# Performance work log

Measured on AMD Instinct MI355X. Metric: run time of the kernel, lower is better.

## Reference

```python
import jax, jax.numpy as jnp
import numpy as np

# _norm_l1l2l3(l1=1, l2=1, l3=2) = 3/4 (computed from the factorial/double-factorial formula)
NORM = 0.75

N, IN1, IN2, KOUT = 512, 128, 128, 128


def setup_inputs() -> dict:
    key = jax.random.key(0)
    k1, k2, k3 = jax.random.split(key, 3)
    x = jax.random.normal(k1, (N, 3, IN1), dtype=jnp.float32)
    y = jax.random.normal(k2, (N, 3, IN2), dtype=jnp.float32)
    w = jax.random.normal(k3, (IN1, IN2, KOUT), dtype=jnp.float32)
    a = jnp.float32(1.0)
    return {"w": w, "a": a, "x": x, "y": y}


def reference(w, a, x, y):
    # contraction1: outer product over the two Cartesian axes (l1=1, l2=1 -> l3=2)
    # x: [n, i=3, a], y: [n, j=3, b] -> out1: [n, 3, 3, a, b]
    out1 = jnp.einsum("nia,njb->nijab", x, y)
    # contraction2: weighted contraction of feature channels with scaled weights
    # (w*a): [a, b, k], out1: [n, 3, 3, a, b] -> [n, 3, 3, k]
    out2 = NORM * jnp.einsum("abk,nijab->nijk", w * a, out1)
    return (out1, out2)
```

## Files before the change

kernel.cpp:

```cpp
#include <hip/hip_runtime.h>
#include <stdint.h>

typedef __attribute__((ext_vector_type(8))) short bf16x8;
typedef __attribute__((ext_vector_type(4))) float f32x4;

static constexpr int O1_ELEMS    = 512*3*3*128*128;
static constexpr int WB2_FLOATS  = 1048576;
static constexpr size_t SCRATCH_BYTES = (size_t)WB2_FLOATS*4;
static constexpr int NTILES      = 4608;
static constexpr int SKIP_TILES  = 64;
static constexpr int S1          = 512;
static constexpr int NCB         = 384;

__device__ inline unsigned short f32_to_bf16(float f) {
    union { float f; uint32_t u; } v; v.f = f;
    uint32_t r = v.u + 0x7FFF + ((v.u >> 16) & 1);
    return (unsigned short)(r >> 16);
}

__device__ inline bf16x8 bf16x8_from_f32(const float* p) {
    float4 v0 = *(const float4*)p;
    float4 v1 = *(const float4*)(p + 4);
    union { bf16x8 v; unsigned short s[8]; } u;
    u.s[0] = f32_to_bf16(v0.x); u.s[1] = f32_to_bf16(v0.y);
    u.s[2] = f32_to_bf16(v0.z); u.s[3] = f32_to_bf16(v0.w);
    u.s[4] = f32_to_bf16(v1.x); u.s[5] = f32_to_bf16(v1.y);
    u.s[6] = f32_to_bf16(v1.z); u.s[7] = f32_to_bf16(v1.w);
    return u.v;
}

__device__ inline void write_tile(int tile, const float* __restrict__ x,
                                  const float* __restrict__ y,
                                  float* __restrict__ out1, int t) {
    const f32x4* y4 = (const f32x4*)y;
    f32x4* o4 = (f32x4*)out1;
    const int b4 = t & 31, a0 = t >> 5;
    int n  = tile / 9;
    int ij = tile - n * 9;
    int i  = ij / 3, j = ij - i * 3;
    f32x4 yv = y4[(n * 3 + j) * 32 + b4];
    const float* xrow = x + (n * 3 + i) * 128;
    f32x4* dst = o4 + (size_t)tile * 4096 + a0 * 32 + b4;
    #pragma unroll
    for (int p = 0; p < 16; ++p) {
        float xs = xrow[p * 8 + a0];
        f32x4 r = yv * xs;
        __builtin_nontemporal_store(r, dst);
        dst += 256;
    }
}

__device__ inline void conv_role(int a, int t, const float* __restrict__ w,
                                 unsigned short* __restrict__ wb2, char* smem) {
    unsigned short (*lt)[132] = (unsigned short (*)[132])smem;
    const float4* src = (const float4*)(w + (size_t)a * 16384);
    #pragma unroll
    for (int it = 0; it < 16; ++it) {
        int fidx = it * 256 + t;
        float4 v = src[fidx];
        int b = fidx >> 5, k4 = fidx & 31;
        unsigned short* d = &lt[b][k4 * 4];
        d[0] = f32_to_bf16(v.x); d[1] = f32_to_bf16(v.y);
        d[2] = f32_to_bf16(v.z); d[3] = f32_to_bf16(v.w);
    }
    __syncthreads();
    const int k = t >> 1, bh = t & 1;
    uint4* dst = (uint4*)(wb2 + (size_t)a * 16384 + (size_t)k * 128 + bh * 64);
    #pragma unroll
    for (int i8 = 0; i8 < 8; ++i8) {
        uint32_t pk[4];
        #pragma unroll
        for (int q = 0; q < 4; ++q) {
            uint32_t lo = lt[bh * 64 + i8 * 8 + q * 2][k];
            uint32_t hi = lt[bh * 64 + i8 * 8 + q * 2 + 1][k];
            pk[q] = lo | (hi << 16);
        }
        uint4 vv = {pk[0], pk[1], pk[2], pk[3]};
        dst[i8] = vv;
    }
}

__device__ inline void comp_role(int cb, int tid, float alpha,
                                 const float* __restrict__ x,
                                 const float* __restrict__ y,
                                 const unsigned short* __restrict__ wb2,
                                 float* __restrict__ out2, char* smem) {
    float (*xsh)[3][32] = (float (*)[3][32])smem;
    const int ksl = cb & 7;
    const int mt  = cb >> 3;
    const int l   = tid & 63;
    const int wv  = tid >> 6;
    const int l15 = l & 15, lg = l >> 4;

    bf16x8 afrag[2][4];
    #pragma unroll
    for (int Mt = 0; Mt < 2; ++Mt)
        #pragma unroll
        for (int ks = 0; ks < 4; ++ks)
            afrag[Mt][ks] = bf16x8_from_f32(
                y + (size_t)(mt * 32 + Mt * 16 + l15) * 128 + ks * 32 + lg * 8);

    #pragma unroll
    for (int p = 0; p < 48; ++p) {
        int e = tid + p * 256;
        int aa = e / 96, r = e - aa * 96, i = r >> 5, mm = r & 31;
        int n = (mt * 32 + mm) / 3;
        xsh[aa][i][mm] = x[n * 384 + i * 128 + aa];
    }
    __syncthreads();

    float acc2[3][2][4] = {};
    const unsigned short* wbase =
        wb2 + (size_t)(ksl * 16 + l15) * 128 + lg * 8;

    #pragma unroll 2
    for (int ac = 0; ac < 32; ++ac) {
        const int a = wv * 32 + ac;
        const unsigned short* wp = wbase + (size_t)a * 16384;
        bf16x8 bf0 = *(const bf16x8*)(wp);
        bf16x8 bf1 = *(const bf16x8*)(wp + 32);
        bf16x8 bf2 = *(const bf16x8*)(wp + 64);
        bf16x8 bf3 = *(const bf16x8*)(wp + 96);

        f32x4 t0 = {0.f, 0.f, 0.f, 0.f}, t1 = {0.f, 0.f, 0.f, 0.f};
        t0 = __builtin_amdgcn_mfma_f32_16x16x32_bf16(afrag[0][0], bf0, t0, 0, 0, 0);
        t1 = __builtin_amdgcn_mfma_f32_16x16x32_bf16(afrag[1][0], bf0, t1, 0, 0, 0);
        t0 = __builtin_amdgcn_mfma_f32_16x16x32_bf16(afrag[0][1], bf1, t0, 0, 0, 0);
        t1 = __builtin_amdgcn_mfma_f32_16x16x32_bf16(afrag[1][1], bf1, t1, 0, 0, 0);
        t0 = __builtin_amdgcn_mfma_f32_16x16x32_bf16(afrag[0][2], bf2, t0, 0, 0, 0);
        t1 = __builtin_amdgcn_mfma_f32_16x16x32_bf16(afrag[1][2], bf2, t1, 0, 0, 0);
        t0 = __builtin_amdgcn_mfma_f32_16x16x32_bf16(afrag[0][3], bf3, t0, 0, 0, 0);
        t1 = __builtin_amdgcn_mfma_f32_16x16x32_bf16(afrag[1][3], bf3, t1, 0, 0, 0);

        #pragma unroll
        for (int i = 0; i < 3; ++i) {
            float4 xv0 = *(const float4*)&xsh[a][i][lg * 4];
            float4 xv1 = *(const float4*)&xsh[a][i][16 + lg * 4];
            acc2[i][0][0] += xv0.x * t0[0]; acc2[i][0][1] += xv0.y * t0[1];
            acc2[i][0][2] += xv0.z * t0[2]; acc2[i][0][3] += xv0.w * t0[3];
            acc2[i][1][0] += xv1.x * t1[0]; acc2[i][1][1] += xv1.y * t1[1];
            acc2[i][1][2] += xv1.z * t1[2]; acc2[i][1][3] += xv1.w * t1[3];
        }
    }

    __syncthreads();
    float* red = (float*)smem;
    const int base = (wv * 64 + l) * 24;
    #pragma unroll
    for (int i = 0; i < 3; ++i)
        #pragma unroll
        for (int Mt = 0; Mt < 2; ++Mt)
            #pragma unroll
            for (int r = 0; r < 4; ++r)
                red[base + (i * 2 + Mt) * 4 + r] = acc2[i][Mt][r];
    __syncthreads();

    if (wv == 0) {
        #pragma unroll
        for (int i = 0; i < 3; ++i)
            #pragma unroll
            for (int Mt = 0; Mt < 2; ++Mt)
                #pragma unroll
                for (int r = 0; r < 4; ++r) {
                    const int idx = (i * 2 + Mt) * 4 + r;
                    float s = acc2[i][Mt][r]
                            + red[(64 + l) * 24 + idx]
                            + red[(128 + l) * 24 + idx]
                            + red[(192 + l) * 24 + idx];
                    int m = mt * 32 + Mt * 16 + lg * 4 + r;
                    int n = m / 3, j = m - 3 * n;
                    out2[((size_t)(n * 3 + i) * 3 + j) * 128 + ksl * 16 + l15] =
                        alpha * s;
                }
    }
}

__global__ __launch_bounds__(256) void k1_kernel(const float* __restrict__ w,
                                                 const float* __restrict__ x,
                                                 const float* __restrict__ y,
                                                 unsigned short* __restrict__ wb2,
                                                 float* __restrict__ out1, int t0) {
    __shared__ __align__(16) char smem[33792];
    const int b = (int)blockIdx.x;
    if (b < 128) { conv_role(b, (int)threadIdx.x, w, wb2, smem); return; }
    write_tile(t0 + b - 128, x, y, out1, (int)threadIdx.x);
}

__global__ __launch_bounds__(256) void k2_kernel(const float* __restrict__ a_s,
                                                 const float* __restrict__ x,
                                                 const float* __restrict__ y,
                                                 const unsigned short* __restrict__ wb2,
                                                 float* __restrict__ out1,
                                                 float* __restrict__ out2, int t0) {
    __shared__ __align__(16) char smem[49152];
    const int b = (int)blockIdx.x;
    const int t = (int)threadIdx.x;
    if (b < NCB) {
        comp_role(b, t, 0.75f * a_s[0], x, y, wb2, out2, smem);
        return;
    }
    write_tile(t0 + S1 + (b - NCB), x, y, out1, t);
}

__global__ __launch_bounds__(256) void finish_kernel(const float* __restrict__ x,
                                                     const float* __restrict__ y,
                                                     float* __restrict__ out1) {
    write_tile((int)blockIdx.x, x, y, out1, (int)threadIdx.x);
}

extern "C" void kernel_launch(void* const* d_in, const int* in_sizes, int n_in,
                              void* d_out, int out_size, void* d_ws, size_t ws_size,
                              hipStream_t stream) {
    const float* w  = (const float*)d_in[0];
    const float* as = (const float*)d_in[1];
    const float* x  = (const float*)d_in[2];
    const float* y  = (const float*)d_in[3];
    float* out1 = (float*)d_out;
    float* out2 = out1 + O1_ELEMS;

    const bool have_ws = (ws_size >= SCRATCH_BYTES);
    unsigned short* wb2 = have_ws ? (unsigned short*)d_ws : (unsigned short*)out1;
    const int t0 = have_ws ? 0 : SKIP_TILES;
    const int s2 = NTILES - t0 - S1;

    k1_kernel<<<128 + S1, 256, 0, stream>>>(w, x, y, wb2, out1, t0);
    k2_kernel<<<NCB + s2, 256, 0, stream>>>(as, x, y, wb2, out1, out2, t0);
    if (!have_ws)
        finish_kernel<<<SKIP_TILES, 256, 0, stream>>>(x, y, out1);
}
```

Baseline: 69.75 us.

## Fuse weight conversion into compute by gathering fp32 weights directly into MFMA fragments

Removes the separate bf16 transpose/convert pass over w and its scratch buffer, so the whole op becomes a single kernel launch. Compute blocks now read fp32 weights with strided scalar loads (stride 128 floats) and convert to bf16 in registers inside the MFMA loop. This drops one launch and a kernel boundary but replaces vector 16-byte loads with eight uncoalesced-per-lane scalar gathers per fragment, which increases load instructions and L2 traffic in the hot loop.

```diff
diff --git a/kernel.cpp b/kernel.cpp
--- a/kernel.cpp
+++ b/kernel.cpp
@@ -4,13 +4,9 @@
 typedef __attribute__((ext_vector_type(8))) short bf16x8;
 typedef __attribute__((ext_vector_type(4))) float f32x4;
 
-static constexpr int O1_ELEMS    = 512*3*3*128*128;
-static constexpr int WB2_FLOATS  = 1048576;
-static constexpr size_t SCRATCH_BYTES = (size_t)WB2_FLOATS*4;
-static constexpr int NTILES      = 4608;
-static constexpr int SKIP_TILES  = 64;
-static constexpr int S1          = 512;
-static constexpr int NCB         = 384;
+static constexpr int O1_ELEMS = 512*3*3*128*128;
+static constexpr int NTILES   = 4608;
+static constexpr int NCB      = 384;
 
 __device__ inline unsigned short f32_to_bf16(float f) {
     union { float f; uint32_t u; } v; v.f = f;
@@ -26,6 +22,13 @@
     u.s[2] = f32_to_bf16(v0.z); u.s[3] = f32_to_bf16(v0.w);
     u.s[4] = f32_to_bf16(v1.x); u.s[5] = f32_to_bf16(v1.y);
     u.s[6] = f32_to_bf16(v1.z); u.s[7] = f32_to_bf16(v1.w);
+    return u.v;
+}
+
+__device__ inline bf16x8 gather_bf16(const float* __restrict__ p) {
+    union { bf16x8 v; unsigned short s[8]; } u;
+    #pragma unroll
+    for (int q = 0; q < 8; ++q) u.s[q] = f32_to_bf16(p[q * 128]);
     return u.v;
 }
 
@@ -50,40 +53,10 @@
     }
 }
 
-__device__ inline void conv_role(int a, int t, const float* __restrict__ w,
-                                 unsigned short* __restrict__ wb2, char* smem) {
-    unsigned short (*lt)[132] = (unsigned short (*)[132])smem;
-    const float4* src = (const float4*)(w + (size_t)a * 16384);
-    #pragma unroll
-    for (int it = 0; it < 16; ++it) {
-        int fidx = it * 256 + t;
-        float4 v = src[fidx];
-        int b = fidx >> 5, k4 = fidx & 31;
-        unsigned short* d = &lt[b][k4 * 4];
-        d[0] = f32_to_bf16(v.x); d[1] = f32_to_bf16(v.y);
-        d[2] = f32_to_bf16(v.z); d[3] = f32_to_bf16(v.w);
-    }
-    __syncthreads();
-    const int k = t >> 1, bh = t & 1;
-    uint4* dst = (uint4*)(wb2 + (size_t)a * 16384 + (size_t)k * 128 + bh * 64);
-    #pragma unroll
-    for (int i8 = 0; i8 < 8; ++i8) {
-        uint32_t pk[4];
-        #pragma unroll
-        for (int q = 0; q < 4; ++q) {
-            uint32_t lo = lt[bh * 64 + i8 * 8 + q * 2][k];
-            uint32_t hi = lt[bh * 64 + i8 * 8 + q * 2 + 1][k];
-            pk[q] = lo | (hi << 16);
-        }
-        uint4 vv = {pk[0], pk[1], pk[2], pk[3]};
-        dst[i8] = vv;
-    }
-}
-
 __device__ inline void comp_role(int cb, int tid, float alpha,
                                  const float* __restrict__ x,
                                  const float* __restrict__ y,
-                                 const unsigned short* __restrict__ wb2,
+                                 const float* __restrict__ w,
                                  float* __restrict__ out2, char* smem) {
     float (*xsh)[3][32] = (float (*)[3][32])smem;
     const int ksl = cb & 7;
@@ -110,17 +83,16 @@
     __syncthreads();
 
     float acc2[3][2][4] = {};
-    const unsigned short* wbase =
-        wb2 + (size_t)(ksl * 16 + l15) * 128 + lg * 8;
+    const float* wgb = w + (size_t)(lg * 8) * 128 + ksl * 16 + l15;
 
     #pragma unroll 2
     for (int ac = 0; ac < 32; ++ac) {
         const int a = wv * 32 + ac;
-        const unsigned short* wp = wbase + (size_t)a * 16384;
-        bf16x8 bf0 = *(const bf16x8*)(wp);
-        bf16x8 bf1 = *(const bf16x8*)(wp + 32);
-        bf16x8 bf2 = *(const bf16x8*)(wp + 64);
-        bf16x8 bf3 = *(const bf16x8*)(wp + 96);
+        const float* wp = wgb + (size_t)a * 16384;
+        bf16x8 bf0 = gather_bf16(wp);
+        bf16x8 bf1 = gather_bf16(wp + 32 * 128);
+        bf16x8 bf2 = gather_bf16(wp + 64 * 128);
+        bf16x8 bf3 = gather_bf16(wp + 96 * 128);
 
         f32x4 t0 = {0.f, 0.f, 0.f, 0.f}, t1 = {0.f, 0.f, 0.f, 0.f};
         t0 = __builtin_amdgcn_mfma_f32_16x16x32_bf16(afrag[0][0], bf0, t0, 0, 0, 0);
@@ -175,37 +147,20 @@
     }
 }
 
-__global__ __launch_bounds__(256) void k1_kernel(const float* __restrict__ w,
-                                                 const float* __restrict__ x,
-                                                 const float* __restrict__ y,
-                                                 unsigned short* __restrict__ wb2,
-                                                 float* __restrict__ out1, int t0) {
-    __shared__ __align__(16) char smem[33792];
-    const int b = (int)blockIdx.x;
-    if (b < 128) { conv_role(b, (int)threadIdx.x, w, wb2, smem); return; }
-    write_tile(t0 + b - 128, x, y, out1, (int)threadIdx.x);
-}
-
-__global__ __launch_bounds__(256) void k2_kernel(const float* __restrict__ a_s,
-                                                 const float* __restrict__ x,
-                                                 const float* __restrict__ y,
-                                                 const unsigned short* __restrict__ wb2,
-                                                 float* __restrict__ out1,
-                                                 float* __restrict__ out2, int t0) {
+__global__ __launch_bounds__(256) void mega_kernel(const float* __restrict__ a_s,
+                                                   const float* __restrict__ w,
+                                                   const float* __restrict__ x,
+                                                   const float* __restrict__ y,
+                                                   float* __restrict__ out1,
+                                                   float* __restrict__ out2) {
     __shared__ __align__(16) char smem[49152];
     const int b = (int)blockIdx.x;
     const int t = (int)threadIdx.x;
     if (b < NCB) {
-        comp_role(b, t, 0.75f * a_s[0], x, y, wb2, out2, smem);
+        comp_role(b, t, 0.75f * a_s[0], x, y, w, out2, smem);
         return;
     }
-    write_tile(t0 + S1 + (b - NCB), x, y, out1, t);
-}
-
-__global__ __launch_bounds__(256) void finish_kernel(const float* __restrict__ x,
-                                                     const float* __restrict__ y,
-                                                     float* __restrict__ out1) {
-    write_tile((int)blockIdx.x, x, y, out1, (int)threadIdx.x);
+    write_tile(b - NCB, x, y, out1, t);
 }
 
 extern "C" void kernel_launch(void* const* d_in, const int* in_sizes, int n_in,
@@ -218,13 +173,5 @@
     float* out1 = (float*)d_out;
     float* out2 = out1 + O1_ELEMS;
 
-    const bool have_ws = (ws_size >= SCRATCH_BYTES);
-    unsigned short* wb2 = have_ws ? (unsigned short*)d_ws : (unsigned short*)out1;
-    const int t0 = have_ws ? 0 : SKIP_TILES;
-    const int s2 = NTILES - t0 - S1;
-
-    k1_kernel<<<128 + S1, 256, 0, stream>>>(w, x, y, wb2, out1, t0);
-    k2_kernel<<<NCB + s2, 256, 0, stream>>>(as, x, y, wb2, out1, out2, t0);
-    if (!have_ws)
-        finish_kernel<<<SKIP_TILES, 256, 0, stream>>>(x, y, out1);
+    mega_kernel<<<NCB + NTILES, 256, 0, stream>>>(as, w, x, y, out1, out2);
 }
```

Measured after the change: 94.96 us. 1.36x slower.
